# Optimization experiments

Hardware: AMD Instinct MI355X
Metric: run time of the kernel (lower is better)

The kernel has to match this reference:

```python
import jax, jax.numpy as jnp
import numpy as np

B, N, M, K, D, DO = 4, 32768, 8192, 16, 128, 128


def setup_inputs() -> dict:
    key = jax.random.key(0)
    ks = jax.random.split(key, 8)
    return dict(
        xyz=jax.random.normal(ks[0], (B, N, 3), jnp.float32),
        x=jax.random.normal(ks[1], (B, D, N), jnp.float32),
        xyz_center=jax.random.normal(ks[2], (B, M, 3), jnp.float32),
        idx=jax.random.randint(ks[3], (B, M, K), 0, N, jnp.int32),
        alpha=jnp.ones((1,), jnp.float32),
        beta=jnp.ones((1,), jnp.float32),
        norm_radius=jnp.ones((1,), jnp.float32),
        w1=jax.random.normal(ks[4], (K, 3), jnp.float32) * 0.1,
        g1=jnp.ones((K,), jnp.float32),
        b1=jnp.zeros((K,), jnp.float32),
        w2=jax.random.normal(ks[5], (K, 2 * K), jnp.float32) * 0.1,
        g2=jnp.ones((K,), jnp.float32),
        b2=jnp.zeros((K,), jnp.float32),
        w3=jax.random.normal(ks[6], (K, 2 * K), jnp.float32) * 0.1,
        cv_w=jax.random.normal(ks[7], (DO, D, K), jnp.float32) * 0.02,
    )


def _inorm(t, g, b, eps=1e-5):
    # InstanceNorm2d: normalize each (batch, channel) plane over spatial dims (m, k)
    mu = t.mean(axis=(2, 3), keepdims=True)
    var = t.var(axis=(2, 3), keepdims=True)
    return (t - mu) * jax.lax.rsqrt(var + eps) * g[None, :, None, None] + b[None, :, None, None]


def reference(xyz, x, xyz_center, idx, alpha, beta, norm_radius, w1, g1, b1, w2, g2, b2, w3, cv_w):
    k = idx.shape[-1]
    gather = jax.vmap(lambda pts, i: pts[i])  # per-batch gather
    xyz_group = gather(xyz, idx)                      # b m k 3
    x_group = gather(jnp.swapaxes(x, 1, 2), idx)      # b m k d

    pts = xyz_group - xyz_center[:, :, None, :]       # b m k 3
    # dist computed on detached pts (torch .detach())
    dist = jnp.sqrt(jnp.sum(jnp.square(jax.lax.stop_gradient(pts)), -1))  # b m k
    mean_radius = dist.max(-1).mean()
    nr = norm_radius * 0.9 + mean_radius * 0.1        # EMA-updated radius (non-trainable)
    pts = pts / nr

    dw = jax.nn.sigmoid(-alpha * dist + beta)         # b m k
    s = dw.sum(-1, keepdims=True)
    s = s + (s == 0).astype(dw.dtype) + 1e-6
    dw = dw / s * k
    dw4 = dw[:, None, :, :]                           # b 1 m k

    ptsT = jnp.transpose(pts, (0, 3, 1, 2))           # b 3 m k
    mat = jax.nn.relu(_inorm(jnp.einsum('bcmk,oc->bomk', ptsT, w1), g1, b1))
    mp1 = jnp.broadcast_to((mat * dw4).max(-1, keepdims=True), mat.shape)
    mat = jax.nn.relu(_inorm(jnp.einsum('bcmk,oc->bomk', jnp.concatenate([mat, mp1], 1), w2), g2, b2))
    mp2 = jnp.broadcast_to((mat * dw4).max(-1, keepdims=True), mat.shape)
    mat = jax.nn.relu(jnp.einsum('bcmk,oc->bomk', jnp.concatenate([mat, mp2], 1), w3)) * dw4

    out = jnp.einsum('bmkd,bjmk->bdmj', x_group, mat)  # b d m k
    out = jnp.einsum('bdmj,odj->bom', out, cv_w)
    return out
```

## Files before the change

kernel.cpp:

```cpp
#include <hip/hip_runtime.h>
#include <hip/hip_bf16.h>

#define BB 4
#define NN 32768
#define MM 8192
#define KK 16
#define DD 128
#define DOUT 128
#define TT 2048

typedef unsigned short ushortT;
typedef unsigned int uintT;
typedef __attribute__((ext_vector_type(8))) short short8;
typedef __attribute__((ext_vector_type(4))) float f32x4;
typedef __attribute__((ext_vector_type(2))) float f32x2;

__device__ __forceinline__ ushortT f2bf(float f) {
  union { float f; uintT u; } v; v.f = f;
  uintT u = v.u;
  return (ushortT)((u + 0x7FFFu + ((u >> 16) & 1u)) >> 16);
}

#define ST_MAXD 0
#define ST_E1 16
#define ST_A1 160
#define ST_B1 224
#define ST_E2 288
#define ST_A2 416
#define ST_B2 480

__global__ __launch_bounds__(256) void kxT(const float* __restrict__ x, ushortT* __restrict__ xTb) {
  __shared__ float tile[32][33];
  const int b = blockIdx.z;
  const int n0 = blockIdx.x * 32, d0 = blockIdx.y * 32;
  const int tx = threadIdx.x, ty = threadIdx.y;
  const float* xp = x + (size_t)b * DD * NN;
  #pragma unroll
  for (int i = 0; i < 4; i++)
    tile[ty + i * 8][tx] = xp[(size_t)(d0 + ty + i * 8) * NN + n0 + tx];
  __syncthreads();
  ushortT* op = xTb + (size_t)b * NN * DD;
  #pragma unroll
  for (int i = 0; i < 4; i++)
    op[(size_t)(n0 + ty + i * 8) * DD + d0 + tx] = f2bf(tile[tx][ty + i * 8]);
}

__global__ __launch_bounds__(256) void kWb(const float* __restrict__ cw, ushortT* __restrict__ wb) {
  const int i = blockIdx.x * 256 + threadIdx.x;
  wb[i] = f2bf(cw[i]);
}

__global__ __launch_bounds__(256) void kpassA(const float* __restrict__ xyz,
    const float* __restrict__ xyzc, const int* __restrict__ idx,
    const float* __restrict__ w1, float* __restrict__ st, float4* __restrict__ pts4) {
  const int b = blockIdx.y;
  const int tid = threadIdx.x;
  const int mloc = tid >> 4, k = tid & 15;
  const int m = blockIdx.x * 16 + mloc;
  const int gi = (b * MM + m) * KK + k;
  const int n = idx[gi];
  const float cx = xyzc[(b * MM + m) * 3 + 0];
  const float cy = xyzc[(b * MM + m) * 3 + 1];
  const float cz = xyzc[(b * MM + m) * 3 + 2];
  const float* p = xyz + ((size_t)b * NN + n) * 3;
  const float px = p[0] - cx, py = p[1] - cy, pz = p[2] - cz;
  const float dist = sqrtf(px * px + py * py + pz * pz);
  pts4[gi] = (float4){px, py, pz, dist};
  float maxd = dist;
  maxd = fmaxf(maxd, __shfl_xor(maxd, 1));
  maxd = fmaxf(maxd, __shfl_xor(maxd, 2));
  maxd = fmaxf(maxd, __shfl_xor(maxd, 4));
  maxd = fmaxf(maxd, __shfl_xor(maxd, 8));
  __shared__ float red[16];
  __shared__ float wred[4][32];
  if (k == 0) red[mloc] = maxd;
  float vs[16], vq[16];
  #pragma unroll
  for (int o = 0; o < 16; o++) {
    float e = px * w1[3 * o] + py * w1[3 * o + 1] + pz * w1[3 * o + 2];
    vs[o] = e; vq[o] = e * e;
  }
  #pragma unroll
  for (int s = 1; s < 64; s <<= 1) {
    #pragma unroll
    for (int o = 0; o < 16; o++) {
      vs[o] += __shfl_xor(vs[o], s);
      vq[o] += __shfl_xor(vq[o], s);
    }
  }
  const int wv = tid >> 6, lane = tid & 63;
  if (lane == 0) {
    #pragma unroll
    for (int o = 0; o < 16; o++) { wred[wv][o] = vs[o]; wred[wv][16 + o] = vq[o]; }
  }
  __syncthreads();
  if (tid < 32) {
    float a = wred[0][tid] + wred[1][tid] + wred[2][tid] + wred[3][tid];
    atomicAdd(&st[ST_E1 + b * 32 + tid], a);
  }
  if (tid == 0) {
    float s = 0.f;
    #pragma unroll
    for (int i = 0; i < 16; i++) s += red[i];
    atomicAdd(&st[ST_MAXD], s);
  }
}

__global__ void kS1(const float* __restrict__ nrad, const float* __restrict__ g1,
                    const float* __restrict__ b1, float* __restrict__ st) {
  const int tid = threadIdx.x;
  if (tid >= 64) return;
  const float meanrad = st[ST_MAXD] / (float)(BB * MM);
  const float nr = nrad[0] * 0.9f + meanrad * 0.1f;
  const int b = tid >> 4, o = tid & 15;
  const float cnt = (float)(MM * KK);
  const float sum = st[ST_E1 + b * 32 + o];
  const float sq  = st[ST_E1 + b * 32 + 16 + o];
  const float mu = sum / cnt;
  float var = sq / cnt - mu * mu; var = fmaxf(var, 0.f);
  const float invs = rsqrtf(var + 1e-5f * nr * nr);
  const float a = invs * g1[o];
  st[ST_A1 + b * 16 + o] = a;
  st[ST_B1 + b * 16 + o] = b1[o] - mu * a;
}

__global__ __launch_bounds__(256) void kpassB(const float4* __restrict__ pts4,
    const float* __restrict__ alpha, const float* __restrict__ beta,
    const float* __restrict__ w1, const float* __restrict__ w2,
    float* __restrict__ st) {
  const int b = blockIdx.y;
  const int tid = threadIdx.x;
  __shared__ float w2s[512];
  __shared__ float wred[4][32];
  w2s[tid] = w2[tid]; w2s[256 + tid] = w2[256 + tid];
  const int gi = b * MM * KK + blockIdx.x * 256 + tid;
  const float4 p4 = pts4[gi];
  const float px = p4.x, py = p4.y, pz = p4.z, dist = p4.w;
  float dwv = 1.f / (1.f + expf(alpha[0] * dist - beta[0]));
  float s = dwv;
  s += __shfl_xor(s, 1); s += __shfl_xor(s, 2); s += __shfl_xor(s, 4); s += __shfl_xor(s, 8);
  s = s + (s == 0.f ? 1.f : 0.f) + 1e-6f;
  dwv = dwv / s * 16.f;
  float mat1[16], mp1[16];
  #pragma unroll
  for (int o = 0; o < 16; o++) {
    float e = px * w1[3 * o] + py * w1[3 * o + 1] + pz * w1[3 * o + 2];
    float v = e * st[ST_A1 + b * 16 + o] + st[ST_B1 + b * 16 + o];
    mat1[o] = fmaxf(v, 0.f);
    float t = mat1[o] * dwv;
    t = fmaxf(t, __shfl_xor(t, 1)); t = fmaxf(t, __shfl_xor(t, 2));
    t = fmaxf(t, __shfl_xor(t, 4)); t = fmaxf(t, __shfl_xor(t, 8));
    mp1[o] = t;
  }
  __syncthreads();
  float vs[16], vq[16];
  #pragma unroll
  for (int o = 0; o < 16; o++) {
    float acc = 0.f;
    #pragma unroll
    for (int c = 0; c < 16; c++)
      acc += mat1[c] * w2s[o * 32 + c] + mp1[c] * w2s[o * 32 + 16 + c];
    vs[o] = acc; vq[o] = acc * acc;
  }
  #pragma unroll
  for (int s2 = 1; s2 < 64; s2 <<= 1) {
    #pragma unroll
    for (int o = 0; o < 16; o++) {
      vs[o] += __shfl_xor(vs[o], s2);
      vq[o] += __shfl_xor(vq[o], s2);
    }
  }
  const int wv = tid >> 6, lane = tid & 63;
  if (lane == 0) {
    #pragma unroll
    for (int o = 0; o < 16; o++) { wred[wv][o] = vs[o]; wred[wv][16 + o] = vq[o]; }
  }
  __syncthreads();
  if (tid < 32) {
    float a = wred[0][tid] + wred[1][tid] + wred[2][tid] + wred[3][tid];
    atomicAdd(&st[ST_E2 + b * 32 + tid], a);
  }
}

__global__ void kS2(const float* __restrict__ g2, const float* __restrict__ b2,
                    float* __restrict__ st) {
  const int tid = threadIdx.x;
  if (tid >= 64) return;
  const int b = tid >> 4, o = tid & 15;
  const float cnt = (float)(MM * KK);
  const float sum = st[ST_E2 + b * 32 + o];
  const float sq  = st[ST_E2 + b * 32 + 16 + o];
  const float mu = sum / cnt;
  float var = sq / cnt - mu * mu; var = fmaxf(var, 0.f);
  const float invs = rsqrtf(var + 1e-5f);
  const float a = invs * g2[o];
  st[ST_A2 + b * 16 + o] = a;
  st[ST_B2 + b * 16 + o] = b2[o] - mu * a;
}

__global__ __launch_bounds__(512, 4) void kF1(const float4* __restrict__ pts4,
    const int* __restrict__ idx,
    const float* __restrict__ alpha, const float* __restrict__ beta,
    const float* __restrict__ w1, const float* __restrict__ w2, const float* __restrict__ w3,
    const float* __restrict__ st, const ushortT* __restrict__ xTb, ushortT* __restrict__ Aout) {
  __shared__ float mat3s[32 * 256];
  const int b = blockIdx.y;
  const int tid = threadIdx.x;
  const int m0 = blockIdx.x * 32;

  const int mloc = tid >> 4, k1 = tid & 15;
  const int gi = (b * MM + m0) * KK + tid;
  const float4 p4 = pts4[gi];
  const float px = p4.x, py = p4.y, pz = p4.z, dist = p4.w;
  float dwv = 1.f / (1.f + expf(alpha[0] * dist - beta[0]));
  {
    float s = dwv;
    s += __shfl_xor(s, 1); s += __shfl_xor(s, 2); s += __shfl_xor(s, 4); s += __shfl_xor(s, 8);
    s = s + (s == 0.f ? 1.f : 0.f) + 1e-6f;
    dwv = dwv / s * 16.f;
  }

  f32x2 v1[16];
  #pragma unroll
  for (int o = 0; o < 16; o++) {
    float e = px * w1[3 * o] + py * w1[3 * o + 1] + pz * w1[3 * o + 2];
    float v = e * st[ST_A1 + b * 16 + o] + st[ST_B1 + b * 16 + o];
    v = fmaxf(v, 0.f);
    float t = v * dwv;
    t = fmaxf(t, __shfl_xor(t, 1)); t = fmaxf(t, __shfl_xor(t, 2));
    t = fmaxf(t, __shfl_xor(t, 4)); t = fmaxf(t, __shfl_xor(t, 8));
    if (o & 1) { v1[o >> 1].y = v; v1[8 + (o >> 1)].y = t; }
    else       { v1[o >> 1].x = v; v1[8 + (o >> 1)].x = t; }
  }

  const int wid = __builtin_amdgcn_readfirstlane(tid >> 6);
  const int lane = tid & 63;
  const int jh = lane >> 5;
  const int dq = lane & 31;
  const int d0 = dq * 4;
  const int jq0 = jh * 2;
  const ushortT* xb = xTb + (size_t)b * NN * DD + d0;

  uint2 xA[16], xB[16];

#define PREF(dst, gg) do {                                                 \
    const int* ib = idx + (((b * MM + m0 + (gg) * 8 + wid)) << 4);         \
    _Pragma("unroll")                                                      \
    for (int k = 0; k < 16; k++) {                                         \
      const uintT nn = (uintT)ib[k];                                       \
      (dst)[k] = *(const uint2*)(xb + ((size_t)nn << 7));                  \
    }                                                                      \
  } while (0)

  PREF(xA, 0);

  {
    float in2[16];
    #pragma unroll
    for (int o = 0; o < 16; o++) {
      f32x2 acc = {0.f, 0.f};
      #pragma unroll
      for (int cp = 0; cp < 16; cp++) {
        const f32x2 wv = *(const f32x2*)(w2 + o * 32 + 2 * cp);
        acc += v1[cp] * wv;
      }
      float v = (acc.x + acc.y) * st[ST_A2 + b * 16 + o] + st[ST_B2 + b * 16 + o];
      in2[o] = fmaxf(v, 0.f);
    }
    f32x2 v2[16];
    #pragma unroll
    for (int o = 0; o < 16; o++) {
      float t = in2[o] * dwv;
      t = fmaxf(t, __shfl_xor(t, 1)); t = fmaxf(t, __shfl_xor(t, 2));
      t = fmaxf(t, __shfl_xor(t, 4)); t = fmaxf(t, __shfl_xor(t, 8));
      if (o & 1) { v2[o >> 1].y = in2[o]; v2[8 + (o >> 1)].y = t; }
      else       { v2[o >> 1].x = in2[o]; v2[8 + (o >> 1)].x = t; }
    }
    float m3v[16];
    #pragma unroll
    for (int j = 0; j < 16; j++) {
      f32x2 acc = {0.f, 0.f};
      #pragma unroll
      for (int cp = 0; cp < 16; cp++) {
        const f32x2 wv = *(const f32x2*)(w3 + j * 32 + 2 * cp);
        acc += v2[cp] * wv;
      }
      m3v[j] = fmaxf(acc.x + acc.y, 0.f) * dwv;
    }
    const int swz1 = (k1 ^ (k1 >> 2)) & 3;
    float* m3w = &mat3s[mloc * 256 + k1 * 16];
    #pragma unroll
    for (int q = 0; q < 4; q++)
      *(f32x4*)(m3w + ((q ^ swz1) << 2)) =
          (f32x4){m3v[4 * q], m3v[4 * q + 1], m3v[4 * q + 2], m3v[4 * q + 3]};
  }
  __syncthreads();

#define COMP(src, gg) do {                                                 \
    const int ml = (gg) * 8 + wid;                                         \
    const float* m3base = &mat3s[ml * 256];                                \
    f32x2 a2[4][4];                                                        \
    _Pragma("unroll")                                                      \
    for (int d = 0; d < 4; d++)                                            \
      _Pragma("unroll")                                                    \
      for (int c = 0; c < 4; c++) a2[d][c] = (f32x2){0.f, 0.f};            \
    _Pragma("unroll")                                                      \
    for (int k = 0; k < 16; k++) {                                         \
      const int sw = (k ^ (k >> 2)) & 3;                                   \
      const uint2 xv = (src)[k];                                           \
      const f32x4 mq0 = *(const f32x4*)(m3base + k * 16 + ((jq0 ^ sw) << 2));        \
      const f32x4 mq1 = *(const f32x4*)(m3base + k * 16 + (((jq0 + 1) ^ sw) << 2));  \
      float xs[4];                                                         \
      xs[0] = __uint_as_float(xv.x << 16);                                 \
      xs[1] = __uint_as_float(xv.x & 0xFFFF0000u);                         \
      xs[2] = __uint_as_float(xv.y << 16);                                 \
      xs[3] = __uint_as_float(xv.y & 0xFFFF0000u);                         \
      f32x2 mp[4];                                                         \
      mp[0] = mq0.lo; mp[1] = mq0.hi;                                      \
      mp[2] = mq1.lo; mp[3] = mq1.hi;                                      \
      _Pragma("unroll")                                                    \
      for (int d = 0; d < 4; d++) {                                        \
        const float xd = xs[d];                                            \
        _Pragma("unroll")                                                  \
        for (int c = 0; c < 4; c++)                                        \
          a2[d][c] += mp[c] * xd;                                          \
      }                                                                    \
    }                                                                      \
    ushortT* aop = Aout + ((size_t)b * MM + m0 + ml) * TT + d0 * 16 + jh * 8;  \
    _Pragma("unroll")                                                      \
    for (int d = 0; d < 4; d++) {                                          \
      uintT u[4];                                                          \
      _Pragma("unroll")                                                    \
      for (int c = 0; c < 4; c++)                                          \
        u[c] = (uintT)f2bf(a2[d][c].x) | ((uintT)f2bf(a2[d][c].y) << 16);  \
      *(uint4*)(aop + d * 16) = (uint4){u[0], u[1], u[2], u[3]};           \
    }                                                                      \
  } while (0)

  PREF(xB, 1);
  COMP(xA, 0);
  PREF(xA, 2);
  COMP(xB, 1);
  PREF(xB, 3);
  COMP(xA, 2);
  COMP(xB, 3);

#undef PREF
#undef COMP
}

__global__ __launch_bounds__(512) void kgemm(const ushortT* __restrict__ Wb,
                                             const ushortT* __restrict__ Aout,
                                             float* __restrict__ out) {
  __shared__ ushortT At[128 * 40];
  __shared__ ushortT Bt[128 * 40];
  const int b = blockIdx.y;
  const int m0 = blockIdx.x * 128;
  const int tid = threadIdx.x;
  const int w = tid >> 6, l = tid & 63;
  const int ow = (w >> 2) * 64, mw = (w & 3) * 32;
  const int fr = l & 15, fg = l >> 4;
  f32x4 acc[4][2];
  #pragma unroll
  for (int i = 0; i < 4; i++)
    #pragma unroll
    for (int j = 0; j < 2; j++)
      acc[i][j] = (f32x4){0.f, 0.f, 0.f, 0.f};
  const int srow = tid >> 2, sk = (tid & 3) * 8;
  const ushortT* wp = Wb + srow * TT + sk;
  const ushortT* ap = Aout + ((size_t)b * MM + m0 + srow) * TT + sk;
  for (int k0 = 0; k0 < TT; k0 += 32) {
    uint4 wv = *(const uint4*)(wp + k0);
    uint4 av = *(const uint4*)(ap + k0);
    *(uint4*)&At[srow * 40 + sk] = wv;
    *(uint4*)&Bt[srow * 40 + sk] = av;
    __syncthreads();
    short8 a[4], bfrag[2];
    #pragma unroll
    for (int i = 0; i < 4; i++) a[i] = *(short8*)&At[(ow + i * 16 + fr) * 40 + fg * 8];
    #pragma unroll
    for (int j = 0; j < 2; j++) bfrag[j] = *(short8*)&Bt[(mw + j * 16 + fr) * 40 + fg * 8];
    #pragma unroll
    for (int i = 0; i < 4; i++)
      #pragma unroll
      for (int j = 0; j < 2; j++)
        acc[i][j] = __builtin_amdgcn_mfma_f32_16x16x32_bf16(a[i], bfrag[j], acc[i][j], 0, 0, 0);
    __syncthreads();
  }
  #pragma unroll
  for (int i = 0; i < 4; i++)
    #pragma unroll
    for (int j = 0; j < 2; j++)
      #pragma unroll
      for (int r = 0; r < 4; r++) {
        const int o = ow + i * 16 + fg * 4 + r;
        const int m = m0 + mw + j * 16 + fr;
        out[((size_t)b * DOUT + o) * MM + m] = acc[i][j][r];
      }
}

#define XTB_OFF 0
#define PTS_OFF 33554432
#define AOUT_OFF 67108864
#define WB_OFF 201326592
#define ST_OFF 201850880

extern "C" void kernel_launch(void* const* d_in, const int* in_sizes, int n_in,
                              void* d_out, int out_size, void* d_ws, size_t ws_size,
                              hipStream_t stream) {
  const float* xyz  = (const float*)d_in[0];
  const float* x    = (const float*)d_in[1];
  const float* xyzc = (const float*)d_in[2];
  const int*   idx  = (const int*)d_in[3];
  const float* alpha = (const float*)d_in[4];
  const float* beta  = (const float*)d_in[5];
  const float* nrad  = (const float*)d_in[6];
  const float* w1 = (const float*)d_in[7];
  const float* g1 = (const float*)d_in[8];
  const float* b1 = (const float*)d_in[9];
  const float* w2 = (const float*)d_in[10];
  const float* g2 = (const float*)d_in[11];
  const float* b2 = (const float*)d_in[12];
  const float* w3 = (const float*)d_in[13];
  const float* cvw = (const float*)d_in[14];
  char* ws = (char*)d_ws;
  ushortT* xTb  = (ushortT*)(ws + XTB_OFF);
  float4*  pts4 = (float4*)(ws + PTS_OFF);
  ushortT* Aout = (ushortT*)(ws + AOUT_OFF);
  ushortT* Wb   = (ushortT*)(ws + WB_OFF);
  float*   st   = (float*)(ws + ST_OFF);
  float* out = (float*)d_out;

  hipMemsetAsync(st, 0, 4096, stream);
  kxT<<<dim3(NN / 32, DD / 32, BB), dim3(32, 8), 0, stream>>>(x, xTb);
  kWb<<<dim3(DOUT * TT / 256), 256, 0, stream>>>(cvw, Wb);
  kpassA<<<dim3(MM / 16, BB), 256, 0, stream>>>(xyz, xyzc, idx, w1, st, pts4);
  kS1<<<1, 64, 0, stream>>>(nrad, g1, b1, st);
  kpassB<<<dim3(MM / 16, BB), 256, 0, stream>>>(pts4, alpha, beta, w1, w2, st);
  kS2<<<1, 64, 0, stream>>>(g2, b2, st);
  kF1<<<dim3(MM / 32, BB), 512, 0, stream>>>(pts4, idx, alpha, beta, w1, w2, w3, st, xTb, Aout);
  kgemm<<<dim3(MM / 128, BB), 512, 0, stream>>>(Wb, Aout, out);
}
```

Before: 211.6 us.

## Split mat3 MLP into separate kernel and drop LDS weight staging in passB

```diff
diff --git a/kernel.cpp b/kernel.cpp
--- a/kernel.cpp
+++ b/kernel.cpp
@@ -130,9 +130,7 @@
     float* __restrict__ st) {
   const int b = blockIdx.y;
   const int tid = threadIdx.x;
-  __shared__ float w2s[512];
   __shared__ float wred[4][32];
-  w2s[tid] = w2[tid]; w2s[256 + tid] = w2[256 + tid];
   const int gi = b * MM * KK + blockIdx.x * 256 + tid;
   const float4 p4 = pts4[gi];
   const float px = p4.x, py = p4.y, pz = p4.z, dist = p4.w;
@@ -141,26 +139,29 @@
   s += __shfl_xor(s, 1); s += __shfl_xor(s, 2); s += __shfl_xor(s, 4); s += __shfl_xor(s, 8);
   s = s + (s == 0.f ? 1.f : 0.f) + 1e-6f;
   dwv = dwv / s * 16.f;
-  float mat1[16], mp1[16];
+  f32x2 v1[16];
   #pragma unroll
   for (int o = 0; o < 16; o++) {
     float e = px * w1[3 * o] + py * w1[3 * o + 1] + pz * w1[3 * o + 2];
     float v = e * st[ST_A1 + b * 16 + o] + st[ST_B1 + b * 16 + o];
-    mat1[o] = fmaxf(v, 0.f);
-    float t = mat1[o] * dwv;
+    v = fmaxf(v, 0.f);
+    float t = v * dwv;
     t = fmaxf(t, __shfl_xor(t, 1)); t = fmaxf(t, __shfl_xor(t, 2));
     t = fmaxf(t, __shfl_xor(t, 4)); t = fmaxf(t, __shfl_xor(t, 8));
-    mp1[o] = t;
-  }
-  __syncthreads();
+    if (o & 1) { v1[o >> 1].y = v; v1[8 + (o >> 1)].y = t; }
+    else       { v1[o >> 1].x = v; v1[8 + (o >> 1)].x = t; }
+  }
   float vs[16], vq[16];
   #pragma unroll
   for (int o = 0; o < 16; o++) {
-    float acc = 0.f;
-    #pragma unroll
-    for (int c = 0; c < 16; c++)
-      acc += mat1[c] * w2s[o * 32 + c] + mp1[c] * w2s[o * 32 + 16 + c];
-    vs[o] = acc; vq[o] = acc * acc;
+    f32x2 acc = {0.f, 0.f};
+    #pragma unroll
+    for (int cp = 0; cp < 16; cp++) {
+      const f32x2 wv = *(const f32x2*)(w2 + o * 32 + 2 * cp);
+      acc += v1[cp] * wv;
+    }
+    const float e = acc.x + acc.y;
+    vs[o] = e; vq[o] = e * e;
   }
   #pragma unroll
   for (int s2 = 1; s2 < 64; s2 <<= 1) {
@@ -198,20 +199,24 @@
   st[ST_B2 + b * 16 + o] = b2[o] - mu * a;
 }
 
-__global__ __launch_bounds__(512, 4) void kF1(const float4* __restrict__ pts4,
-    const int* __restrict__ idx,
+__global__ __launch_bounds__(256, 6) void kMat3(const float* __restrict__ xyz,
+    const float* __restrict__ xyzc, const int* __restrict__ idx,
     const float* __restrict__ alpha, const float* __restrict__ beta,
-    const float* __restrict__ w1, const float* __restrict__ w2, const float* __restrict__ w3,
-    const float* __restrict__ st, const ushortT* __restrict__ xTb, ushortT* __restrict__ Aout) {
-  __shared__ float mat3s[32 * 256];
+    const float* __restrict__ w1, const float* __restrict__ w2,
+    const float* __restrict__ w3, const float* __restrict__ st,
+    float* __restrict__ mat3g) {
   const int b = blockIdx.y;
   const int tid = threadIdx.x;
-  const int m0 = blockIdx.x * 32;
-
   const int mloc = tid >> 4, k1 = tid & 15;
-  const int gi = (b * MM + m0) * KK + tid;
-  const float4 p4 = pts4[gi];
-  const float px = p4.x, py = p4.y, pz = p4.z, dist = p4.w;
+  const int m = blockIdx.x * 16 + mloc;
+  const int gi = (b * MM + m) * KK + k1;
+  const int n = idx[gi];
+  const float cx = xyzc[(b * MM + m) * 3 + 0];
+  const float cy = xyzc[(b * MM + m) * 3 + 1];
+  const float cz = xyzc[(b * MM + m) * 3 + 2];
+  const float* p = xyz + ((size_t)b * NN + n) * 3;
+  const float px = p[0] - cx, py = p[1] - cy, pz = p[2] - cz;
+  const float dist = sqrtf(px * px + py * py + pz * pz);
   float dwv = 1.f / (1.f + expf(alpha[0] * dist - beta[0]));
   {
     float s = dwv;
@@ -219,7 +224,6 @@
     s = s + (s == 0.f ? 1.f : 0.f) + 1e-6f;
     dwv = dwv / s * 16.f;
   }
-
   f32x2 v1[16];
   #pragma unroll
   for (int o = 0; o < 16; o++) {
@@ -232,6 +236,53 @@
     if (o & 1) { v1[o >> 1].y = v; v1[8 + (o >> 1)].y = t; }
     else       { v1[o >> 1].x = v; v1[8 + (o >> 1)].x = t; }
   }
+  float in2[16];
+  #pragma unroll
+  for (int o = 0; o < 16; o++) {
+    f32x2 acc = {0.f, 0.f};
+    #pragma unroll
+    for (int cp = 0; cp < 16; cp++) {
+      const f32x2 wv = *(const f32x2*)(w2 + o * 32 + 2 * cp);
+      acc += v1[cp] * wv;
+    }
+    float v = (acc.x + acc.y) * st[ST_A2 + b * 16 + o] + st[ST_B2 + b * 16 + o];
+    in2[o] = fmaxf(v, 0.f);
+  }
+  f32x2 v2[16];
+  #pragma unroll
+  for (int o = 0; o < 16; o++) {
+    float t = in2[o] * dwv;
+    t = fmaxf(t, __shfl_xor(t, 1)); t = fmaxf(t, __shfl_xor(t, 2));
+    t = fmaxf(t, __shfl_xor(t, 4)); t = fmaxf(t, __shfl_xor(t, 8));
+    if (o & 1) { v2[o >> 1].y = in2[o]; v2[8 + (o >> 1)].y = t; }
+    else       { v2[o >> 1].x = in2[o]; v2[8 + (o >> 1)].x = t; }
+  }
+  float m3v[16];
+  #pragma unroll
+  for (int j = 0; j < 16; j++) {
+    f32x2 acc = {0.f, 0.f};
+    #pragma unroll
+    for (int cp = 0; cp < 16; cp++) {
+      const f32x2 wv = *(const f32x2*)(w3 + j * 32 + 2 * cp);
+      acc += v2[cp] * wv;
+    }
+    m3v[j] = fmaxf(acc.x + acc.y, 0.f) * dwv;
+  }
+  const int swz1 = (k1 ^ (k1 >> 2)) & 3;
+  float* m3w = mat3g + (((size_t)b * MM + blockIdx.x * 16) << 8) + tid * 16;
+  #pragma unroll
+  for (int q = 0; q < 4; q++)
+    *(f32x4*)(m3w + ((q ^ swz1) << 2)) =
+        (f32x4){m3v[4 * q], m3v[4 * q + 1], m3v[4 * q + 2], m3v[4 * q + 3]};
+}
+
+__global__ __launch_bounds__(512, 4) void kF2(const int* __restrict__ idx,
+    const float* __restrict__ mat3g, const ushortT* __restrict__ xTb,
+    ushortT* __restrict__ Aout) {
+  __shared__ float mat3s[32 * 256];
+  const int b = blockIdx.y;
+  const int tid = threadIdx.x;
+  const int m0 = blockIdx.x * 32;
 
   const int wid = __builtin_amdgcn_readfirstlane(tid >> 6);
   const int lane = tid & 63;
@@ -255,44 +306,11 @@
   PREF(xA, 0);
 
   {
-    float in2[16];
-    #pragma unroll
-    for (int o = 0; o < 16; o++) {
-      f32x2 acc = {0.f, 0.f};
-      #pragma unroll
-      for (int cp = 0; cp < 16; cp++) {
-        const f32x2 wv = *(const f32x2*)(w2 + o * 32 + 2 * cp);
-        acc += v1[cp] * wv;
-      }
-      float v = (acc.x + acc.y) * st[ST_A2 + b * 16 + o] + st[ST_B2 + b * 16 + o];
-      in2[o] = fmaxf(v, 0.f);
-    }
-    f32x2 v2[16];
-    #pragma unroll
-    for (int o = 0; o < 16; o++) {
-      float t = in2[o] * dwv;
-      t = fmaxf(t, __shfl_xor(t, 1)); t = fmaxf(t, __shfl_xor(t, 2));
-      t = fmaxf(t, __shfl_xor(t, 4)); t = fmaxf(t, __shfl_xor(t, 8));
-      if (o & 1) { v2[o >> 1].y = in2[o]; v2[8 + (o >> 1)].y = t; }
-      else       { v2[o >> 1].x = in2[o]; v2[8 + (o >> 1)].x = t; }
-    }
-    float m3v[16];
-    #pragma unroll
-    for (int j = 0; j < 16; j++) {
-      f32x2 acc = {0.f, 0.f};
-      #pragma unroll
-      for (int cp = 0; cp < 16; cp++) {
-        const f32x2 wv = *(const f32x2*)(w3 + j * 32 + 2 * cp);
-        acc += v2[cp] * wv;
-      }
-      m3v[j] = fmaxf(acc.x + acc.y, 0.f) * dwv;
-    }
-    const int swz1 = (k1 ^ (k1 >> 2)) & 3;
-    float* m3w = &mat3s[mloc * 256 + k1 * 16];
+    const float* src = mat3g + (((size_t)b * MM + m0) << 8) + tid * 16;
+    float* dst = &mat3s[tid * 16];
     #pragma unroll
     for (int q = 0; q < 4; q++)
-      *(f32x4*)(m3w + ((q ^ swz1) << 2)) =
-          (f32x4){m3v[4 * q], m3v[4 * q + 1], m3v[4 * q + 2], m3v[4 * q + 3]};
+      *(f32x4*)(dst + q * 4) = *(const f32x4*)(src + q * 4);
   }
   __syncthreads();
 
@@ -401,6 +419,7 @@
 
 #define XTB_OFF 0
 #define PTS_OFF 33554432
+#define MAT3_OFF 33554432
 #define AOUT_OFF 67108864
 #define WB_OFF 201326592
 #define ST_OFF 201850880
@@ -426,6 +445,7 @@
   char* ws = (char*)d_ws;
   ushortT* xTb  = (ushortT*)(ws + XTB_OFF);
   float4*  pts4 = (float4*)(ws + PTS_OFF);
+  float*   mat3g = (float*)(ws + MAT3_OFF);
   ushortT* Aout = (ushortT*)(ws + AOUT_OFF);
   ushortT* Wb   = (ushortT*)(ws + WB_OFF);
   float*   st   = (float*)(ws + ST_OFF);
@@ -438,6 +458,7 @@
   kS1<<<1, 64, 0, stream>>>(nrad, g1, b1, st);
   kpassB<<<dim3(MM / 16, BB), 256, 0, stream>>>(pts4, alpha, beta, w1, w2, st);
   kS2<<<1, 64, 0, stream>>>(g2, b2, st);
-  kF1<<<dim3(MM / 32, BB), 512, 0, stream>>>(pts4, idx, alpha, beta, w1, w2, w3, st, xTb, Aout);
+  kMat3<<<dim3(MM / 16, BB), 256, 0, stream>>>(xyz, xyzc, idx, alpha, beta, w1, w2, w3, st, mat3g);
+  kF2<<<dim3(MM / 32, BB), 512, 0, stream>>>(idx, mat3g, xTb, Aout);
   kgemm<<<dim3(MM / 128, BB), 512, 0, stream>>>(Wb, Aout, out);
 }
```

After: 222.7 us. +5.3%, slower.
